# Optimization experiments

Hardware: AMD Instinct MI355X
Metric: run time of the kernel (lower is better)

Reference implementation:

```python
import jax, jax.numpy as jnp
import numpy as np
import math

NUM_HEADS = 16
HEAD_DIM = 64
D_MODEL = NUM_HEADS * HEAD_DIM  # 1024
B, S = 4, 2048

def setup_inputs() -> dict:
    key = jax.random.key(0)
    ks = jax.random.split(key, 8)
    sd = 1.0 / math.sqrt(D_MODEL)
    return {
        "hidden_states": jax.random.normal(ks[0], (B, S, D_MODEL), jnp.float32),
        "attention_mask": jnp.zeros((B, 1, 1, S), jnp.float32),
        "Wq": jax.random.normal(ks[1], (D_MODEL, D_MODEL), jnp.float32) * sd,
        "bq": jnp.zeros((D_MODEL,), jnp.float32),
        "Wk": jax.random.normal(ks[2], (D_MODEL, D_MODEL), jnp.float32) * sd,
        "bk": jnp.zeros((D_MODEL,), jnp.float32),
        "Wv": jax.random.normal(ks[3], (D_MODEL, D_MODEL), jnp.float32) * sd,
        "bv": jnp.zeros((D_MODEL,), jnp.float32),
    }

def _split_heads(x):
    # [B, S, D] -> [B, H, S, hd]
    b, s, _ = x.shape
    return x.reshape(b, s, NUM_HEADS, HEAD_DIM).transpose(0, 2, 1, 3)

def reference(hidden_states, attention_mask, Wq, bq, Wk, bk, Wv, bv):
    # Linear projections (torch nn.Linear: x @ W.T + b)
    q = _split_heads(hidden_states @ Wq.T + bq)
    k = _split_heads(hidden_states @ Wk.T + bk)
    v = _split_heads(hidden_states @ Wv.T + bv)
    scale = 1.0 / math.sqrt(HEAD_DIM)
    # [B, H, Sq, Sk] attention scores, fully materialized as in the original
    scores = jnp.einsum("bhqd,bhkd->bhqk", q, k) * scale + attention_mask
    # relusq replacement for softmax
    probs = jnp.square(jax.nn.relu(scores))
    ctx = jnp.einsum("bhqk,bhkd->bhqd", probs, v)  # [B, H, S, hd]
    b = ctx.shape[0]
    return ctx.transpose(0, 2, 1, 3).reshape(b, -1, D_MODEL)
```

## Files before the change

### kernel.cpp

```cpp
#include <hip/hip_runtime.h>


typedef __bf16 bf16x8 __attribute__((ext_vector_type(8)));
typedef __bf16 bf16x4 __attribute__((ext_vector_type(4)));
typedef short  s16x4  __attribute__((ext_vector_type(4)));
typedef float  f32x4  __attribute__((ext_vector_type(4)));
typedef float  floatx4 __attribute__((ext_vector_type(4)));

#define MFMA16(a, b, c) __builtin_amdgcn_mfma_f32_16x16x32_bf16(a, b, c, 0, 0, 0)
#define MFMA16K16(a, b, c) \
    __builtin_amdgcn_mfma_f32_16x16x16bf16_1k(a, b, c, 0, 0, 0)

#define WAITCNT_VM4() __builtin_amdgcn_s_waitcnt(0x0F74)

__device__ __forceinline__ void glds16(const __bf16* g, __bf16* l) {
    __builtin_amdgcn_global_load_lds(
        (const __attribute__((address_space(1))) void*)g,
        (__attribute__((address_space(3))) void*)l, 16, 0, 0);
}

__global__ __launch_bounds__(256) void convert_kernel(
    const float* __restrict__ X, const float* __restrict__ Wq,
    const float* __restrict__ Wk, const float* __restrict__ Wv,
    __bf16* __restrict__ Xb, __bf16* __restrict__ Wqb,
    __bf16* __restrict__ Wkb, __bf16* __restrict__ Wvb)
{
    int blk = blockIdx.x;
    const float* src; __bf16* dst; size_t base;
    if (blk < 4096)      { src = X;  dst = Xb;  base = (size_t)blk * 2048; }
    else if (blk < 4608) { src = Wq; dst = Wqb; base = (size_t)(blk - 4096) * 2048; }
    else if (blk < 5120) { src = Wk; dst = Wkb; base = (size_t)(blk - 4608) * 2048; }
    else                 { src = Wv; dst = Wvb; base = (size_t)(blk - 5120) * 2048; }
    size_t off = base + (size_t)threadIdx.x * 8;
    floatx4 a = *(const floatx4*)(src + off);
    floatx4 c = *(const floatx4*)(src + off + 4);
    bf16x8 o;
    o[0] = (__bf16)a[0]; o[1] = (__bf16)a[1]; o[2] = (__bf16)a[2]; o[3] = (__bf16)a[3];
    o[4] = (__bf16)c[0]; o[5] = (__bf16)c[1]; o[6] = (__bf16)c[2]; o[7] = (__bf16)c[3];
    *(bf16x8*)(dst + off) = o;
}

__global__ __launch_bounds__(256) void qkv_gemm_kernel(
    const __bf16* __restrict__ Xb,
    const __bf16* __restrict__ Wqb, const __bf16* __restrict__ Wkb,
    const __bf16* __restrict__ Wvb,
    const float* __restrict__ bq, const float* __restrict__ bk,
    const float* __restrict__ bv,
    __bf16* __restrict__ qws, __bf16* __restrict__ kws, __bf16* __restrict__ vws)
{
    __shared__ __bf16 As[128 * 64];
    __shared__ __bf16 Bs[128 * 64];

    const int tid  = threadIdx.x;
    const int lane = tid & 63;
    const int wave = tid >> 6;
    const int wm   = (wave >> 1) * 64;
    const int wn   = (wave & 1) * 64;
    const int quad = lane >> 4;
    const int l16  = lane & 15;
    const int m0   = blockIdx.y * 128;

    const int sel = blockIdx.x >> 3;
    const bool vmode = (sel == 2);
    const __bf16* Wb = (sel == 0) ? Wqb : (sel == 1) ? Wkb : Wvb;
    const float* bias = (sel == 0) ? bq : (sel == 1) ? bk : bv;
    __bf16* outp = (sel == 0) ? qws : (sel == 1) ? kws : vws;
    const int n0 = (blockIdx.x & 7) * 128;

    const __bf16* Pa = vmode ? As : Bs;
    const __bf16* Pb = vmode ? Bs : As;
    const int woffA = vmode ? wm : wn;
    const int woffB = vmode ? wn : wm;

    f32x4 acc[4][4] = {};

    for (int k0 = 0; k0 < 1024; k0 += 64) {
        __syncthreads();
        #pragma unroll
        for (int i = 0; i < 4; ++i) {
            int r = wave * 32 + i * 8 + (lane >> 3);
            int c = (lane & 7) ^ (r & 7);
            glds16(Xb + (size_t)(m0 + r) * 1024 + k0 + c * 8,
                   &As[(wave * 32 + i * 8) * 64]);
            glds16(Wb + (size_t)(n0 + r) * 1024 + k0 + c * 8,
                   &Bs[(wave * 32 + i * 8) * 64]);
        }
        __syncthreads();

        #pragma unroll
        for (int kk8 = 0; kk8 < 8; kk8 += 4) {
            bf16x8 af[4], bfr[4];
            #pragma unroll
            for (int a = 0; a < 4; ++a)
                af[a] = *(const bf16x8*)&Pa[(woffA + a * 16 + l16) * 64 +
                                            (((kk8 + quad) ^ (l16 & 7)) * 8)];
            #pragma unroll
            for (int bb = 0; bb < 4; ++bb)
                bfr[bb] = *(const bf16x8*)&Pb[(woffB + bb * 16 + l16) * 64 +
                                              (((kk8 + quad) ^ (l16 & 7)) * 8)];
            #pragma unroll
            for (int a = 0; a < 4; ++a)
                #pragma unroll
                for (int bb = 0; bb < 4; ++bb)
                    acc[a][bb] = MFMA16(af[a], bfr[bb], acc[a][bb]);
        }
    }

    if (!vmode) {
        #pragma unroll
        for (int a = 0; a < 4; ++a) {
            int n = n0 + woffA + a * 16 + quad * 4;
            floatx4 bv4 = *(const floatx4*)&bias[n];
            int h = n >> 6, d0 = n & 63;
            #pragma unroll
            for (int bb = 0; bb < 4; ++bb) {
                int m = m0 + woffB + bb * 16 + l16;
                int bt = m >> 11, s = m & 2047;
                bf16x4 o;
                #pragma unroll
                for (int r = 0; r < 4; ++r)
                    o[r] = (__bf16)(acc[a][bb][r] + bv4[r]);
                *(bf16x4*)&outp[((size_t)(bt * 16 + h) * 2048 + s) * 64 + d0] = o;
            }
        }
    } else {
        #pragma unroll
        for (int a = 0; a < 4; ++a) {
            int m = m0 + woffA + a * 16 + quad * 4;
            int bt = m >> 11, s0 = m & 2047;
            #pragma unroll
            for (int bb = 0; bb < 4; ++bb) {
                int n = n0 + woffB + bb * 16 + l16;
                float bvv = bias[n];
                int h = n >> 6, d = n & 63;
                bf16x4 o;
                #pragma unroll
                for (int r = 0; r < 4; ++r)
                    o[r] = (__bf16)(acc[a][bb][r] + bvv);
                *(bf16x4*)&outp[((size_t)(bt * 16 + h) * 64 + d) * 2048 + s0] = o;
            }
        }
    }
}

__global__ __launch_bounds__(256, 2) void attn_kernel(
    const __bf16* __restrict__ Q, const __bf16* __restrict__ K,
    const __bf16* __restrict__ Vt, const float* __restrict__ mask,
    float* __restrict__ out)
{
    __shared__ __bf16 Ks[2][64 * 64];
    __shared__ __bf16 Vs[2][64 * 64];

    const int tid  = threadIdx.x;
    const int lane = tid & 63;
    const int wave = tid >> 6;
    const int quad = lane >> 4;
    const int l16  = lane & 15;
    const int bh   = blockIdx.y;
    const int b    = bh >> 4;
    const int h    = bh & 15;
    const int q0   = blockIdx.x * 256 + wave * 64;

    const __bf16* Qb = Q  + (size_t)bh * 2048 * 64;
    const __bf16* Kb = K  + (size_t)bh * 2048 * 64;
    const __bf16* Vb = Vt + (size_t)bh * 64 * 2048;
    const float*  mb = mask + b * 2048;

    const int srow = (lane >> 3);
    const int schk = (lane & 7);

    bf16x8 aq[4][2];
    #pragma unroll
    for (int qi = 0; qi < 4; ++qi)
        #pragma unroll
        for (int kcd = 0; kcd < 2; ++kcd)
            aq[qi][kcd] = *(const bf16x8*)(Qb +
                (size_t)(q0 + qi * 16 + l16) * 64 + kcd * 32 + quad * 8);

    f32x4 co[4][4] = {};

    #pragma unroll
    for (int i = 0; i < 2; ++i) {
        int rb = wave * 16 + i * 8;
        int r  = rb + srow;
        int c  = schk ^ (r & 7);
        glds16(Kb + (size_t)r * 64 + c * 8, &Ks[0][rb * 64]);
        glds16(Vb + (size_t)r * 2048 + 0 + c * 8, &Vs[0][rb * 64]);
    }

    for (int t = 0; t < 32; ++t) {
        const int k0 = t * 64;
        const int kn = (k0 + 64) & 2047;
        const int nb = (t + 1) & 1;
        #pragma unroll
        for (int i = 0; i < 2; ++i) {
            int rb = wave * 16 + i * 8;
            int r  = rb + srow;
            int c  = schk ^ (r & 7);
            glds16(Kb + (size_t)(kn + r) * 64 + c * 8, &Ks[nb][rb * 64]);
            glds16(Vb + (size_t)r * 2048 + kn + c * 8, &Vs[nb][rb * 64]);
        }
        WAITCNT_VM4();
        __syncthreads();

        const __bf16* Kt = &Ks[t & 1][0];
        const __bf16* Vtile = &Vs[t & 1][0];

        bf16x4 pf[4][4];
        #pragma unroll
        for (int ki = 0; ki < 4; ++ki) {
            f32x4 st[4] = {};
            #pragma unroll
            for (int kcd = 0; kcd < 2; ++kcd) {
                int key = ki * 16 + l16;
                bf16x8 ak = *(const bf16x8*)&Kt[key * 64 +
                    (((kcd * 4 + quad) ^ (key & 7)) * 8)];
                #pragma unroll
                for (int qi = 0; qi < 4; ++qi)
                    st[qi] = MFMA16(ak, aq[qi][kcd], st[qi]);
            }
            floatx4 mk = *(const floatx4*)&mb[k0 + ki * 16 + quad * 4];
            #pragma unroll
            for (int qi = 0; qi < 4; ++qi) {
                bf16x4 pv;
                #pragma unroll
                for (int r = 0; r < 4; ++r) {
                    float x = st[qi][r] * 0.125f + mk[r];
                    x = fmaxf(x, 0.0f);
                    pv[r] = (__bf16)(x * x);
                }
                pf[ki][qi] = pv;
            }
        }

        #pragma unroll
        for (int ki = 0; ki < 4; ++ki) {
            bf16x4 vb[4];
            #pragma unroll
            for (int dt = 0; dt < 4; ++dt) {
                int d = dt * 16 + l16;
                int g = ki * 2 + (quad >> 1);
                vb[dt] = *(const bf16x4*)&Vtile[d * 64 +
                    ((g ^ (d & 7)) * 8) + (quad & 1) * 4];
            }
            #pragma unroll
            for (int qi = 0; qi < 4; ++qi) {
                s16x4 pa = __builtin_bit_cast(s16x4, pf[ki][qi]);
                #pragma unroll
                for (int dt = 0; dt < 4; ++dt)
                    co[qi][dt] = MFMA16K16(pa,
                        __builtin_bit_cast(s16x4, vb[dt]), co[qi][dt]);
            }
        }
        __syncthreads();
    }

    #pragma unroll
    for (int qi = 0; qi < 4; ++qi)
        #pragma unroll
        for (int r = 0; r < 4; ++r) {
            int q = q0 + qi * 16 + quad * 4 + r;
            float* orow = &out[(((size_t)b * 2048 + q) * 16 + h) * 64];
            #pragma unroll
            for (int dt = 0; dt < 4; ++dt)
                orow[dt * 16 + l16] = co[qi][dt][r];
        }
}

extern "C" void kernel_launch(void* const* d_in, const int* in_sizes, int n_in,
                              void* d_out, int out_size, void* d_ws, size_t ws_size,
                              hipStream_t stream) {
    const float* hidden = (const float*)d_in[0];
    const float* mask   = (const float*)d_in[1];
    const float* Wq     = (const float*)d_in[2];
    const float* bq     = (const float*)d_in[3];
    const float* Wk     = (const float*)d_in[4];
    const float* bk     = (const float*)d_in[5];
    const float* Wv     = (const float*)d_in[6];
    const float* bv     = (const float*)d_in[7];
    float* out = (float*)d_out;

    __bf16* qws = (__bf16*)d_ws;
    __bf16* kws = qws + (size_t)64 * 2048 * 64;
    __bf16* vws = kws + (size_t)64 * 2048 * 64;
    __bf16* Xb  = vws + (size_t)64 * 2048 * 64;
    __bf16* Wqb = Xb  + (size_t)8192 * 1024;
    __bf16* Wkb = Wqb + (size_t)1024 * 1024;
    __bf16* Wvb = Wkb + (size_t)1024 * 1024;

    dim3 blk(256);
    convert_kernel<<<dim3(5632), blk, 0, stream>>>(hidden, Wq, Wk, Wv,
                                                   Xb, Wqb, Wkb, Wvb);
    qkv_gemm_kernel<<<dim3(24, 64), blk, 0, stream>>>(Xb, Wqb, Wkb, Wvb,
                                                      bq, bk, bv, qws, kws, vws);
    attn_kernel<<<dim3(8, 64), blk, 0, stream>>>(qws, kws, vws, mask, out);
}
```

Measured before the change: 274.9 us.

## Split attention key range across two wave groups with shared-memory reduction

Each attention block now runs 512 threads. Two groups of four waves each process half of the key sequence for the same 256 queries, and their partial context accumulators are summed through LDS before the store. This doubles the waves resident per block and halves the serial key loop per wave, aiming at better latency hiding and occupancy on the 512-block grid. The cost is an extra reduction pass through shared memory plus extra barriers, and LDS use per block doubles to 64 KB.

```diff
diff --git a/kernel.cpp b/kernel.cpp
--- a/kernel.cpp
+++ b/kernel.cpp
@@ -143,28 +143,35 @@
     }
 }
 
-__global__ __launch_bounds__(256, 2) void attn_kernel(
+__global__ __launch_bounds__(512, 4) void attn_kernel(
     const __bf16* __restrict__ Q, const __bf16* __restrict__ K,
     const __bf16* __restrict__ Vt, const float* __restrict__ mask,
     float* __restrict__ out)
 {
-    __shared__ __bf16 Ks[2][64 * 64];
-    __shared__ __bf16 Vs[2][64 * 64];
+    __shared__ __bf16 smem[32768];
 
     const int tid  = threadIdx.x;
     const int lane = tid & 63;
     const int wave = tid >> 6;
+    const int qc   = wave & 3;
+    const int kh   = wave >> 2;
     const int quad = lane >> 4;
     const int l16  = lane & 15;
     const int bh   = blockIdx.y;
     const int b    = bh >> 4;
     const int h    = bh & 15;
-    const int q0   = blockIdx.x * 256 + wave * 64;
+    const int q0   = blockIdx.x * 256 + qc * 64;
+    const int kbase = kh * 1024;
 
     const __bf16* Qb = Q  + (size_t)bh * 2048 * 64;
-    const __bf16* Kb = K  + (size_t)bh * 2048 * 64;
-    const __bf16* Vb = Vt + (size_t)bh * 64 * 2048;
-    const float*  mb = mask + b * 2048;
+    const __bf16* Kb = K  + (size_t)bh * 2048 * 64 + (size_t)kbase * 64;
+    const __bf16* Vb = Vt + (size_t)bh * 64 * 2048 + kbase;
+    const float*  mb = mask + b * 2048 + kbase;
+
+    __bf16* Ks0 = smem + (kh * 2 + 0) * 4096;
+    __bf16* Ks1 = smem + (kh * 2 + 1) * 4096;
+    __bf16* Vs0 = smem + 16384 + (kh * 2 + 0) * 4096;
+    __bf16* Vs1 = smem + 16384 + (kh * 2 + 1) * 4096;
 
     const int srow = (lane >> 3);
     const int schk = (lane & 7);
@@ -181,30 +188,31 @@
 
     #pragma unroll
     for (int i = 0; i < 2; ++i) {
-        int rb = wave * 16 + i * 8;
+        int rb = qc * 16 + i * 8;
         int r  = rb + srow;
         int c  = schk ^ (r & 7);
-        glds16(Kb + (size_t)r * 64 + c * 8, &Ks[0][rb * 64]);
-        glds16(Vb + (size_t)r * 2048 + 0 + c * 8, &Vs[0][rb * 64]);
-    }
-
-    for (int t = 0; t < 32; ++t) {
+        glds16(Kb + (size_t)r * 64 + c * 8, Ks0 + rb * 64);
+        glds16(Vb + (size_t)r * 2048 + c * 8, Vs0 + rb * 64);
+    }
+
+    for (int t = 0; t < 16; ++t) {
         const int k0 = t * 64;
-        const int kn = (k0 + 64) & 2047;
-        const int nb = (t + 1) & 1;
+        const int kn = ((t + 1) & 15) * 64;
+        __bf16* Kn = (t & 1) ? Ks0 : Ks1;
+        __bf16* Vn = (t & 1) ? Vs0 : Vs1;
+        const __bf16* Kt    = (t & 1) ? Ks1 : Ks0;
+        const __bf16* Vtile = (t & 1) ? Vs1 : Vs0;
+
         #pragma unroll
         for (int i = 0; i < 2; ++i) {
-            int rb = wave * 16 + i * 8;
+            int rb = qc * 16 + i * 8;
             int r  = rb + srow;
             int c  = schk ^ (r & 7);
-            glds16(Kb + (size_t)(kn + r) * 64 + c * 8, &Ks[nb][rb * 64]);
-            glds16(Vb + (size_t)r * 2048 + kn + c * 8, &Vs[nb][rb * 64]);
+            glds16(Kb + (size_t)(kn + r) * 64 + c * 8, Kn + rb * 64);
+            glds16(Vb + (size_t)r * 2048 + kn + c * 8, Vn + rb * 64);
         }
         WAITCNT_VM4();
         __syncthreads();
-
-        const __bf16* Kt = &Ks[t & 1][0];
-        const __bf16* Vtile = &Vs[t & 1][0];
 
         bf16x4 pf[4][4];
         #pragma unroll
@@ -255,16 +263,38 @@
         __syncthreads();
     }
 
-    #pragma unroll
-    for (int qi = 0; qi < 4; ++qi)
-        #pragma unroll
-        for (int r = 0; r < 4; ++r) {
-            int q = q0 + qi * 16 + quad * 4 + r;
-            float* orow = &out[(((size_t)b * 2048 + q) * 16 + h) * 64];
+    __syncthreads();
+    float* red = (float*)smem;
+    if (kh == 1) {
+        #pragma unroll
+        for (int qi = 0; qi < 4; ++qi)
             #pragma unroll
             for (int dt = 0; dt < 4; ++dt)
-                orow[dt * 16 + l16] = co[qi][dt][r];
-        }
+                *(floatx4*)&red[qc * 4096 + (qi * 4 + dt) * 256 + lane * 4] =
+                    co[qi][dt];
+    }
+    __syncthreads();
+    if (kh == 0) {
+        #pragma unroll
+        for (int qi = 0; qi < 4; ++qi)
+            #pragma unroll
+            for (int dt = 0; dt < 4; ++dt) {
+                floatx4 other =
+                    *(const floatx4*)&red[qc * 4096 + (qi * 4 + dt) * 256 + lane * 4];
+                co[qi][dt][0] += other[0]; co[qi][dt][1] += other[1];
+                co[qi][dt][2] += other[2]; co[qi][dt][3] += other[3];
+            }
+        #pragma unroll
+        for (int qi = 0; qi < 4; ++qi)
+            #pragma unroll
+            for (int r = 0; r < 4; ++r) {
+                int q = q0 + qi * 16 + quad * 4 + r;
+                float* orow = &out[(((size_t)b * 2048 + q) * 16 + h) * 64];
+                #pragma unroll
+                for (int dt = 0; dt < 4; ++dt)
+                    orow[dt * 16 + l16] = co[qi][dt][r];
+            }
+    }
 }
 
 extern "C" void kernel_launch(void* const* d_in, const int* in_sizes, int n_in,
@@ -293,5 +323,5 @@
                                                    Xb, Wqb, Wkb, Wvb);
     qkv_gemm_kernel<<<dim3(24, 64), blk, 0, stream>>>(Xb, Wqb, Wkb, Wvb,
                                                       bq, bk, bv, qws, kws, vws);
-    attn_kernel<<<dim3(8, 64), blk, 0, stream>>>(qws, kws, vws, mask, out);
-}
+    attn_kernel<<<dim3(8, 64), dim3(512), 0, stream>>>(qws, kws, vws, mask, out);
+}
```

After: 533.0 us. 1.94x slower.
